# Kernel tuning notes

Measured on AMD Instinct MI355X. Metric: run time of the kernel, lower is better.

Reference implementation:

```python
import jax, jax.numpy as jnp
import numpy as np
import math

VOCAB, D, L, NC, DC, K, DFF = 50257, 1024, 8, 4096, 256, 8, 4096
B, T = 8, 256

def ternary_ste(w):
    # torch: w_q + (w - w_q).detach() -> forward value == w, grad only via w_q
    alpha = jnp.maximum(jnp.mean(jnp.abs(w)), 1e-5)
    w_q = jnp.clip(jnp.round(w / alpha), -1.0, 1.0)
    return w_q + jax.lax.stop_gradient(w - w_q)

def rmsnorm(x, w):
    return x * jax.lax.rsqrt(jnp.mean(x * x, axis=-1, keepdims=True) + 1e-6) * w

def setup_inputs() -> dict:
    key = jax.random.key(0)
    ks = jax.random.split(key, 16)
    n = lambda k, sh, s: (jax.random.normal(k, sh, dtype=jnp.float32) * s)
    return {
        'tokens': jax.random.randint(ks[0], (B, T), 0, VOCAB),
        'embed': n(ks[1], (VOCAB, D), 0.02),
        'ln_in_w': jnp.ones((D,), jnp.float32),
        'ln_out_w': jnp.ones((D,), jnp.float32),
        'W_route': n(ks[2], (L, NC, D), 0.02),
        'cells': n(ks[3], (L, NC, DC), 0.01),
        'W_in': n(ks[4], (L, D, DC), 0.01),
        'W_out': n(ks[5], (L, DC, D), 0.01),
        'state_decay': jnp.full((L,), 3.0, jnp.float32),
        'state_gate_w': jnp.full((L, D), 0.1, jnp.float32),
        'state_gate_b': jnp.zeros((L, D), jnp.float32),
        'state_scale': jnp.full((L, D), 0.1, jnp.float32),
        'cell_scale': jnp.full((L,), 0.1, jnp.float32),
        'W_ff_gate': n(ks[6], (L, D, DFF), 0.02),
        'W_ff_up': n(ks[7], (L, D, DFF), 0.02),
        'W_ff_down': n(ks[8], (L, DFF, D), 0.02),
        'ff_norm_w': jnp.ones((L, D), jnp.float32),
        'norm_w': jnp.ones((L, D), jnp.float32),
    }

def _layer(x, Wr, cells, Wi, Wo, sd, sgw, sgb, ss, cs, Wg, Wu, Wd, ffn_w, nrm_w):
    Bx, Tx, Dx = x.shape
    # cell memory
    scores = jnp.einsum('btd,cd->btc', x, ternary_ste(Wr)) / math.sqrt(Dx)
    topk_s, topk_i = jax.lax.top_k(scores, K)          # [B,T,K]
    w = jax.nn.softmax(topk_s, axis=-1)
    cell_vals = cells[topk_i]                          # [B,T,K,DC]
    readout = jnp.einsum('btkc,btk->btc', cell_vals, w)
    x_in = jnp.einsum('btd,dc->btc', x, ternary_ste(Wi))
    cell_out = jnp.einsum('btc,cd->btd', readout + x_in, ternary_ste(Wo))
    # running state scan
    gate = jax.nn.sigmoid(x * sgw + sgb)
    updates = gate * x                                  # [B,T,D]
    decay = jnp.clip(jax.nn.sigmoid(sd), 0.01, 0.99)
    def step(h, u):
        h = h * decay + u
        return h, h
    _, states = jax.lax.scan(step, jnp.zeros((Bx, Dx), x.dtype), jnp.swapaxes(updates, 0, 1))
    state_out = jnp.swapaxes(states, 0, 1) * ss
    x = rmsnorm(x + cs * cell_out + state_out, nrm_w)
    # ternary SwiGLU FFN
    h = rmsnorm(x, ffn_w)
    g = jnp.einsum('btd,df->btf', h, ternary_ste(Wg))
    u = jnp.einsum('btd,df->btf', h, ternary_ste(Wu))
    ff = jnp.einsum('btf,fd->btd', jax.nn.silu(g) * u, ternary_ste(Wd))
    return x + ff

def reference(tokens, embed, ln_in_w, ln_out_w, W_route, cells, W_in, W_out,
              state_decay, state_gate_w, state_gate_b, state_scale, cell_scale,
              W_ff_gate, W_ff_up, W_ff_down, ff_norm_w, norm_w):
    h = rmsnorm(embed[tokens], ln_in_w)
    for i in range(L):
        h = _layer(h, W_route[i], cells[i], W_in[i], W_out[i], state_decay[i],
                   state_gate_w[i], state_gate_b[i], state_scale[i], cell_scale[i],
                   W_ff_gate[i], W_ff_up[i], W_ff_down[i], ff_norm_w[i], norm_w[i])
    logits = jnp.einsum('btd,vd->btv', rmsnorm(h, ln_out_w), embed)  # tied head
    return logits
```

## Files before the change

### kernel.cpp

```cpp
#include <hip/hip_runtime.h>
#include <stdint.h>

typedef __attribute__((ext_vector_type(8))) short bf16x8;
typedef __attribute__((ext_vector_type(4))) float f32x4;
typedef unsigned short u16;
typedef unsigned int u32;

#define MTOK 2048
#define DMODEL 1024
#define NCELL 4096
#define DCELL 256
#define DFF 4096
#define NVOCAB 50257
#define VPAD_LD 50304

static __device__ __forceinline__ u16 f2bf(float f) {
  u32 u = __builtin_bit_cast(u32, f);
  u = (u + 0x7FFFu + ((u >> 16) & 1u)) >> 16;
  return (u16)u;
}
static __device__ __forceinline__ u32 pk2(float a, float b) {
  return (u32)f2bf(a) | ((u32)f2bf(b) << 16);
}
static __device__ __forceinline__ float sigm(float x) { return 1.0f / (1.0f + __expf(-x)); }

static __device__ __forceinline__ void glds16(const void* g, void* l) {
  __builtin_amdgcn_global_load_lds(
      (const __attribute__((address_space(1))) void*)g,
      (__attribute__((address_space(3))) void*)l, 16, 0, 0);
}

static __device__ __forceinline__ float blockReduceSum(float v) {
#pragma unroll
  for (int o = 32; o > 0; o >>= 1) v += __shfl_xor(v, o);
  __shared__ float sm[4];
  __syncthreads();
  if ((threadIdx.x & 63) == 0) sm[threadIdx.x >> 6] = v;
  __syncthreads();
  return sm[0] + sm[1] + sm[2] + sm[3];
}

static __device__ __forceinline__ void blockReducePair1024(
    float& a, float& b, float* sm)
{
#pragma unroll
  for (int o = 32; o > 0; o >>= 1) { a += __shfl_xor(a, o); b += __shfl_xor(b, o); }
  int wv = threadIdx.x >> 6;
  if ((threadIdx.x & 63) == 0) { sm[wv * 2] = a; sm[wv * 2 + 1] = b; }
  __syncthreads();
  float ra = 0.f, rb = 0.f;
#pragma unroll
  for (int i = 0; i < 16; ++i) { ra += sm[i * 2]; rb += sm[i * 2 + 1]; }
  __syncthreads();
  a = ra; b = rb;
}

template<int TM, int TN, int EPI>
static __device__ __forceinline__ void v3_body(
    int bid, int T, char* smem,
    const u16* A, const u16* B,
    float* Cf, u16* Cb, const float* Res,
    int NB, int K, int ldc, float alpha)
{
  u16* As = (u16*)smem;
  u16* Bs = (u16*)(smem + TM * 128);
  constexpr int MI = TM / 32;
  constexpr int NI = TN / 32;
  constexpr int ACH = TM / 32;
  constexpr int BCH = TN / 32;
  constexpr int MB = 2048 / TM;
  const int tid = threadIdx.x;
  const int w = (bid & 7) * (T >> 3) + (bid >> 3);
  const int m0 = (w % MB) * TM;
  const int n0 = (w / MB) * TN;
  const int l = tid & 63;
  const int wv = tid >> 6;
  const int wm = wv >> 1, wn = wv & 1;
  const int lr = l & 15, lg = l >> 4;
  const int wbase = tid & ~63;

  f32x4 acc[MI][NI] = {};

  const int row_ = tid >> 3;
  const int kc_ = (tid & 7) << 3;
  const int nk = K >> 6;

  for (int s = 0; s < nk; ++s) {
    const int k0 = s << 6;
#pragma unroll
    for (int c = 0; c < ACH; ++c) {
      int row = c * 32 + row_;
      glds16(&A[(size_t)(m0 + row) * K + k0 + kc_],
             &As[(size_t)(c * 256 + wbase) * 8]);
    }
#pragma unroll
    for (int c = 0; c < BCH; ++c) {
      int row = c * 32 + row_;
      int gr = n0 + row; if (gr > NB - 1) gr = NB - 1;
      glds16(&B[(size_t)gr * K + k0 + kc_],
             &Bs[(size_t)(c * 256 + wbase) * 8]);
    }
    __syncthreads();
#pragma unroll
    for (int kk = 0; kk < 2; ++kk) {
      bf16x8 fa[MI], fb[NI];
#pragma unroll
      for (int mi = 0; mi < MI; ++mi)
        fa[mi] = *(const bf16x8*)&As[(wm * (TM / 2) + mi * 16 + lr) * 64 + kk * 32 + lg * 8];
#pragma unroll
      for (int ni = 0; ni < NI; ++ni)
        fb[ni] = *(const bf16x8*)&Bs[(wn * (TN / 2) + ni * 16 + lr) * 64 + kk * 32 + lg * 8];
#pragma unroll
      for (int mi = 0; mi < MI; ++mi)
#pragma unroll
        for (int ni = 0; ni < NI; ++ni)
          acc[mi][ni] = __builtin_amdgcn_mfma_f32_16x16x32_bf16(fa[mi], fb[ni], acc[mi][ni], 0, 0, 0);
    }
    __syncthreads();
  }

#pragma unroll
  for (int mi = 0; mi < MI; ++mi)
#pragma unroll
    for (int ni = 0; ni < NI; ++ni) {
      int col = n0 + wn * (TN / 2) + ni * 16 + lr;
#pragma unroll
      for (int j = 0; j < 4; ++j) {
        int row = m0 + wm * (TM / 2) + mi * 16 + lg * 4 + j;
        float v = acc[mi][ni][j];
        if constexpr (EPI == 0) {
          Cf[(size_t)row * ldc + col] = v * alpha;
        } else if constexpr (EPI == 1) {
          size_t off = (size_t)row * ldc + col;
          float r = Res[off] + v;
          Cf[off] = r;
          Cb[off] = f2bf(r);
        } else if constexpr (EPI == 2) {
          if (col < NB) Cf[(size_t)row * ldc + col] = v;
        } else if constexpr (EPI == 3) {
          float p = __shfl_xor(v, 1);
          float a = v * sigm(v) * p;
          float a2 = __shfl_xor(a, 2);
          if ((lr & 3) == 0)
            *(u32*)&Cb[(size_t)row * DFF + (col >> 1)] = pk2(a, a2);
        } else {
          __builtin_nontemporal_store(v, &Cf[(size_t)row * ldc + col]);
        }
      }
    }
}

template<int TM, int TN, int EPI>
__global__ __launch_bounds__(256, 3) void k_gemm_v3(
    const u16* __restrict__ A, const u16* __restrict__ B,
    float* __restrict__ Cf, u16* __restrict__ Cb, const float* __restrict__ Res,
    int NB, int K, int ldc, float alpha)
{
  __shared__ __align__(16) char smem[(TM + TN) * 128];
  v3_body<TM, TN, EPI>(blockIdx.x, gridDim.x, smem, A, B, Cf, Cb, Res,
                       NB, K, ldc, alpha);
}

static __device__ __forceinline__ void transpose_body(
    int bid, char* smem,
    const float* Wi, const float* Wo, const float* Wg, const float* Wu,
    const float* Wd, const float* Wr,
    u16* WiT, u16* WoT, u16* WguT, u16* WdT, u16* WrB)
{
  if (bid >= 12800) {
    int i = (bid - 12800) * 256 + threadIdx.x;
    const float4* s = (const float4*)(Wr + (size_t)i * 8);
    float4 a = s[0], b = s[1];
    *(uint4*)(WrB + (size_t)i * 8) =
        make_uint4(pk2(a.x, a.y), pk2(a.z, a.w), pk2(b.x, b.y), pk2(b.z, b.w));
    return;
  }
  const float* src; u16* dst; int R, C, t0, mul, add;
  if (bid < 256)       { src = Wi; dst = WiT;  R = 1024; C = 256;  t0 = bid;        mul = 1; add = 0; }
  else if (bid < 512)  { src = Wo; dst = WoT;  R = 256;  C = 1024; t0 = bid - 256;  mul = 1; add = 0; }
  else if (bid < 4608) { src = Wg; dst = WguT; R = 1024; C = 4096; t0 = bid - 512;  mul = 2; add = 0; }
  else if (bid < 8704) { src = Wu; dst = WguT; R = 1024; C = 4096; t0 = bid - 4608; mul = 2; add = 1; }
  else                 { src = Wd; dst = WdT;  R = 4096; C = 1024; t0 = bid - 8704; mul = 1; add = 0; }
  int tC = C >> 5;
  int r0 = (t0 / tC) << 5, c0 = (t0 % tC) << 5;
  float (*tile)[33] = (float(*)[33])smem;
  int ty = threadIdx.x >> 3;
  int tx = (threadIdx.x & 7) << 2;
  float4 v = *(const float4*)&src[(size_t)(r0 + ty) * C + c0 + tx];
  tile[ty][tx] = v.x; tile[ty][tx + 1] = v.y; tile[ty][tx + 2] = v.z; tile[ty][tx + 3] = v.w;
  __syncthreads();
  float a = tile[tx][ty], b = tile[tx + 1][ty], c = tile[tx + 2][ty], d = tile[tx + 3][ty];
  *(uint2*)&dst[((size_t)(c0 + ty) * mul + add) * R + r0 + tx] = make_uint2(pk2(a, b), pk2(c, d));
}

__global__ void k_transpose_layer(
    const float* __restrict__ Wi, const float* __restrict__ Wo,
    const float* __restrict__ Wg, const float* __restrict__ Wu,
    const float* __restrict__ Wd, const float* __restrict__ Wr,
    u16* __restrict__ WiT, u16* __restrict__ WoT,
    u16* __restrict__ WguT, u16* __restrict__ WdT, u16* __restrict__ WrB)
{
  __shared__ __align__(16) char smem[4224];
  transpose_body(blockIdx.x, smem, Wi, Wo, Wg, Wu, Wd, Wr,
                 WiT, WoT, WguT, WdT, WrB);
}

static __device__ __forceinline__ void gemm64_body(
    const u16* A, const u16* B, float* Cf,
    int m0, int n0, int K, int lda, int ldb, int ldc, char* smem)
{
  u16* As = (u16*)smem;
  u16* Bs = (u16*)(smem + 64 * 64 * 2);
  const int tid = threadIdx.x;
  const int l = tid & 63;
  const int wv = tid >> 6;
  const int wm = wv >> 1, wn = wv & 1;
  const int lr = l & 15, lg = l >> 4;

  uint4 aR[2], bR[2];
  f32x4 acc[2][2] = {};
  const int nk = K >> 6;

  auto loadAB = [&](int k0) {
#pragma unroll
    for (int c = 0; c < 2; ++c) {
      int id = c * 256 + tid;
      int row = id >> 3, kc = (id & 7) << 3;
      aR[c] = *(const uint4*)&A[(size_t)(m0 + row) * lda + k0 + kc];
      bR[c] = *(const uint4*)&B[(size_t)(n0 + row) * ldb + k0 + kc];
    }
  };
  auto stage = [&]() {
#pragma unroll
    for (int c = 0; c < 2; ++c) {
      int id = c * 256 + tid;
      int row = id >> 3, kc = (id & 7) << 3;
      *(uint4*)&As[row * 64 + kc] = aR[c];
      *(uint4*)&Bs[row * 64 + kc] = bR[c];
    }
  };

  loadAB(0);
  for (int s = 0; s < nk; ++s) {
    __syncthreads();
    stage();
    __syncthreads();
    if (s + 1 < nk) loadAB((s + 1) << 6);
#pragma unroll
    for (int kk = 0; kk < 2; ++kk) {
      bf16x8 fa[2], fb[2];
#pragma unroll
      for (int mi = 0; mi < 2; ++mi)
        fa[mi] = *(const bf16x8*)&As[(wm * 32 + mi * 16 + lr) * 64 + kk * 32 + lg * 8];
#pragma unroll
      for (int ni = 0; ni < 2; ++ni)
        fb[ni] = *(const bf16x8*)&Bs[(wn * 32 + ni * 16 + lr) * 64 + kk * 32 + lg * 8];
#pragma unroll
      for (int mi = 0; mi < 2; ++mi)
#pragma unroll
        for (int ni = 0; ni < 2; ++ni)
          acc[mi][ni] = __builtin_amdgcn_mfma_f32_16x16x32_bf16(fa[mi], fb[ni], acc[mi][ni], 0, 0, 0);
    }
  }

#pragma unroll
  for (int mi = 0; mi < 2; ++mi)
#pragma unroll
    for (int ni = 0; ni < 2; ++ni) {
      int col = n0 + wn * 32 + ni * 16 + lr;
#pragma unroll
      for (int j = 0; j < 4; ++j) {
        int row = m0 + wm * 32 + mi * 16 + lg * 4 + j;
        Cf[(size_t)row * ldc + col] = acc[mi][ni][j];
      }
    }
}

__global__ __launch_bounds__(256, 3) void k_gemm64(
    const u16* __restrict__ A, const u16* __restrict__ B,
    float* __restrict__ Cf, int K, int lda, int ldb, int ldc)
{
  __shared__ __align__(16) char smem[16384];
  gemm64_body(A, B, Cf, blockIdx.x * 64, blockIdx.y * 64, K, lda, ldb, ldc, smem);
}

__global__ __launch_bounds__(256, 3) void k_head_fused(
    const u16* __restrict__ x_bf, const u16* __restrict__ WrB,
    float* __restrict__ scores,
    const u16* __restrict__ WiT, float* __restrict__ xin,
    const float* __restrict__ x_f, float* __restrict__ E,
    const float* __restrict__ sgw, const float* __restrict__ sgb,
    const float* __restrict__ sdec)
{
  __shared__ __align__(16) char smem[32768];
  int bid = blockIdx.x;
  if (bid < 512) {
    v3_body<128, 128, 0>(bid, 512, smem, x_bf, WrB, scores, nullptr, nullptr,
                         NCELL, DMODEL, NCELL, 0.03125f);
    return;
  }
  if (bid < 640) {
    int b2 = bid - 512;
    gemm64_body(x_bf, WiT, xin, (b2 & 31) * 64, (b2 >> 5) * 64,
                DMODEL, DMODEL, DMODEL, DCELL, smem);
    return;
  }
  int tid = (bid - 640) * 256 + threadIdx.x;
  int d = tid & 1023, bc = tid >> 10;
  int b = bc >> 4, c = bc & 15;
  float dec = sigm(sdec[0]);
  dec = fminf(fmaxf(dec, 0.01f), 0.99f);
  float gw = sgw[d], gb = sgb[d];
  size_t base = ((size_t)b * 256 + c * 16) * DMODEL + d;
  float h = 0.f;
  for (int t = 0; t < 16; ++t) {
    float xv = x_f[base + (size_t)t * DMODEL];
    h = h * dec + sigm(xv * gw + gb) * xv;
  }
  E[tid] = h;
}

__global__ __launch_bounds__(256, 3) void k_wd_prep(
    const u16* __restrict__ act, const u16* __restrict__ WdT_cur,
    float* __restrict__ x_f, u16* __restrict__ x_bf,
    const float* __restrict__ Wi, const float* __restrict__ Wo,
    const float* __restrict__ Wg, const float* __restrict__ Wu,
    const float* __restrict__ Wd, const float* __restrict__ Wr,
    u16* __restrict__ WiT, u16* __restrict__ WoT,
    u16* __restrict__ WguT, u16* __restrict__ WdT_nxt, u16* __restrict__ WrB)
{
  __shared__ __align__(16) char smem[16384];
  int bid = blockIdx.x;
  if (bid < 512) {
    v3_body<64, 64, 1>(bid, 512, smem, act, WdT_cur, x_f, x_bf, x_f,
                       DMODEL, DFF, DMODEL, 1.0f);
  } else {
    transpose_body(bid - 512, smem, Wi, Wo, Wg, Wu, Wd, Wr,
                   WiT, WoT, WguT, WdT_nxt, WrB);
  }
}

__global__ __launch_bounds__(256) void k_copy_out(
    const float* __restrict__ pad, float* __restrict__ out)
{
  int row = blockIdx.x;
  const float* s = pad + (size_t)row * VPAD_LD;
  float* d = out + (size_t)row * NVOCAB;
  int t = threadIdx.x;
  int head = (int)((16 - (((size_t)d) & 15)) & 15) >> 2;
  if (t < head) d[t] = s[t];
  int nb = (NVOCAB - head) >> 2;
  const float* sb = s + head;
  float* db = d + head;
  for (int i = t; i < nb; i += 256) {
    f32x4 v;
    v.x = __builtin_nontemporal_load(&sb[i * 4 + 0]);
    v.y = __builtin_nontemporal_load(&sb[i * 4 + 1]);
    v.z = __builtin_nontemporal_load(&sb[i * 4 + 2]);
    v.w = __builtin_nontemporal_load(&sb[i * 4 + 3]);
    __builtin_nontemporal_store(v, (f32x4*)&db[i * 4]);
  }
  int t0 = head + nb * 4;
  int rem = NVOCAB - t0;
  if (t < rem) d[t0 + t] = s[t0 + t];
}

__global__ __launch_bounds__(256) void k_cell_fused(
    const float* __restrict__ scores, const float* __restrict__ cells,
    const float* __restrict__ xin, u16* __restrict__ rb)
{
  __shared__ float sw[4][8];
  __shared__ int si[4][8];
  int row0 = blockIdx.x * 4;
  int wvid = threadIdx.x >> 6;
  int row = row0 + wvid;
  int l = threadIdx.x & 63;
  const float* s = scores + (size_t)row * NCELL;
  float v[8]; int ix[8];
#pragma unroll
  for (int i = 0; i < 8; ++i) { v[i] = -3.4e38f; ix[i] = 0x7fffffff; }
  for (int j = 0; j < 64; ++j) {
    float x = s[j * 64 + l];
    if (x > v[7]) {
      v[7] = x; ix[7] = j * 64 + l;
#pragma unroll
      for (int q = 7; q > 0; --q) {
        if (v[q] > v[q - 1]) {
          float tv = v[q]; v[q] = v[q - 1]; v[q - 1] = tv;
          int tt = ix[q]; ix[q] = ix[q - 1]; ix[q - 1] = tt;
        }
      }
    }
  }
  float ov[8]; int oi[8];
#pragma unroll
  for (int r = 0; r < 8; ++r) {
    float bv = v[0]; int bi = ix[0];
#pragma unroll
    for (int o = 32; o > 0; o >>= 1) {
      float tv = __shfl_xor(bv, o);
      int tb = __shfl_xor(bi, o);
      if (tv > bv || (tv == bv && tb < bi)) { bv = tv; bi = tb; }
    }
    ov[r] = bv; oi[r] = bi;
    if (bi == ix[0]) {
#pragma unroll
      for (int q = 0; q < 7; ++q) { v[q] = v[q + 1]; ix[q] = ix[q + 1]; }
      v[7] = -3.4e38f; ix[7] = 0x7fffffff;
    }
  }
  if (l == 0) {
    float m = ov[0], sum = 0.f, e[8];
#pragma unroll
    for (int r = 0; r < 8; ++r) { e[r] = __expf(ov[r] - m); sum += e[r]; }
    float inv = 1.0f / sum;
#pragma unroll
    for (int r = 0; r < 8; ++r) { sw[wvid][r] = e[r] * inv; si[wvid][r] = oi[r]; }
  }
  __syncthreads();
  int d = threadIdx.x;
#pragma unroll
  for (int r = 0; r < 4; ++r) {
    int rr = row0 + r;
    float acc = xin[(size_t)rr * DCELL + d];
#pragma unroll
    for (int k = 0; k < 8; ++k)
      acc += sw[r][k] * cells[(size_t)si[r][k] * DCELL + d];
    rb[(size_t)rr * DCELL + d] = f2bf(acc);
  }
}

__global__ __launch_bounds__(1024) void k_scan_norm(
    float* __restrict__ x_f, const float* __restrict__ co,
    const float* __restrict__ E, u16* __restrict__ h2b,
    const float* __restrict__ sgw, const float* __restrict__ sgb,
    const float* __restrict__ ssc, const float* __restrict__ sdec,
    const float* __restrict__ csc, const float* __restrict__ nw,
    const float* __restrict__ fw)
{
  __shared__ float sm[32];
  int b = blockIdx.x >> 4, c = blockIdx.x & 15;
  int d = threadIdx.x;
  float dec = sigm(sdec[0]);
  dec = fminf(fmaxf(dec, 0.01f), 0.99f);
  float d2 = dec * dec, d4 = d2 * d2, d8 = d4 * d4;
  float d16 = d8 * d8;
  float cs = csc[0];
  float gw = sgw[d], gb = sgb[d], sc = ssc[d];
  float nwd = nw[d], fwd = fw[d];
  float h = 0.f;
  for (int cc = 0; cc < c; ++cc) h = h * d16 + E[((b << 4) + cc) * 1024 + d];
  size_t base = ((size_t)b * 256 + c * 16) * DMODEL + d;
  for (int t = 0; t < 16; ++t) {
    size_t o = base + (size_t)t * DMODEL;
    float xv = x_f[o];
    float g = sigm(xv * gw + gb);
    h = h * dec + g * xv;
    float pre = xv + cs * co[o] + h * sc;
    float pn = pre * nwd;
    float s1 = pre * pre, s2 = pn * pn;
    blockReducePair1024(s1, s2, sm);
    float inv = rsqrtf(s1 * (1.0f / DMODEL) + 1e-6f);
    float x1 = pre * inv * nwd;
    float inv2 = rsqrtf(inv * inv * s2 * (1.0f / DMODEL) + 1e-6f);
    x_f[o] = x1;
    h2b[o] = f2bf(x1 * inv2 * fwd);
  }
}

__global__ void k_embed_norm(const int* __restrict__ tok, const float* __restrict__ emb,
                             const float* __restrict__ w, float* __restrict__ xf,
                             u16* __restrict__ xb)
{
  int row = blockIdx.x;
  int t = tok[row];
  float4 v = ((const float4*)(emb + (size_t)t * DMODEL))[threadIdx.x];
  float tot = blockReduceSum(v.x * v.x + v.y * v.y + v.z * v.z + v.w * v.w);
  float inv = rsqrtf(tot * (1.0f / DMODEL) + 1e-6f);
  int d0 = threadIdx.x << 2;
  float4 wv = *(const float4*)(w + d0);
  float4 o;
  o.x = v.x * inv * wv.x; o.y = v.y * inv * wv.y;
  o.z = v.z * inv * wv.z; o.w = v.w * inv * wv.w;
  *(float4*)(xf + (size_t)row * DMODEL + d0) = o;
  *(uint2*)(xb + (size_t)row * DMODEL + d0) = make_uint2(pk2(o.x, o.y), pk2(o.z, o.w));
}

__global__ __launch_bounds__(256) void k_tail(
    const float* __restrict__ xf, const float* __restrict__ w,
    u16* __restrict__ ob, const float* __restrict__ emb,
    u16* __restrict__ emb_bf)
{
  int bid = blockIdx.x;
  if (bid >= 2048) {
    int i = (bid - 2048) * 256 + threadIdx.x;
    if (i >= NVOCAB * (DMODEL / 8)) return;
    const float4* s = (const float4*)(emb + (size_t)i * 8);
    float4 a = s[0], b = s[1];
    *(uint4*)(emb_bf + (size_t)i * 8) =
        make_uint4(pk2(a.x, a.y), pk2(a.z, a.w), pk2(b.x, b.y), pk2(b.z, b.w));
    return;
  }
  int row = bid;
  float4 v = ((const float4*)(xf + (size_t)row * DMODEL))[threadIdx.x];
  float tot = blockReduceSum(v.x * v.x + v.y * v.y + v.z * v.z + v.w * v.w);
  float inv = rsqrtf(tot * (1.0f / DMODEL) + 1e-6f);
  int d0 = threadIdx.x << 2;
  float4 wv = *(const float4*)(w + d0);
  *(uint2*)(ob + (size_t)row * DMODEL + d0) =
      make_uint2(pk2(v.x * inv * wv.x, v.y * inv * wv.y),
                 pk2(v.z * inv * wv.z, v.w * inv * wv.w));
}

extern "C" void kernel_launch(void* const* d_in, const int* in_sizes, int n_in,
                              void* d_out, int out_size, void* d_ws, size_t ws_size,
                              hipStream_t stream)
{
  const int*   tokens  = (const int*)d_in[0];
  const float* embed   = (const float*)d_in[1];
  const float* ln_in_w = (const float*)d_in[2];
  const float* ln_out_w= (const float*)d_in[3];
  const float* W_route = (const float*)d_in[4];
  const float* cells   = (const float*)d_in[5];
  const float* W_in    = (const float*)d_in[6];
  const float* W_out   = (const float*)d_in[7];
  const float* sdec    = (const float*)d_in[8];
  const float* sgw     = (const float*)d_in[9];
  const float* sgb     = (const float*)d_in[10];
  const float* ssc     = (const float*)d_in[11];
  const float* csc     = (const float*)d_in[12];
  const float* Wg      = (const float*)d_in[13];
  const float* Wu      = (const float*)d_in[14];
  const float* Wd      = (const float*)d_in[15];
  const float* ffw     = (const float*)d_in[16];
  const float* nrw     = (const float*)d_in[17];
  float* out = (float*)d_out;
  (void)in_sizes; (void)n_in; (void)out_size;

  char* ws = (char*)d_ws;
  size_t off = 0;
  auto alloc = [&](size_t bytes) -> void* {
    void* p = ws + off;
    off += (bytes + 255) & ~(size_t)255;
    return p;
  };

  float* scores = (float*)alloc((size_t)MTOK * NCELL * 4);
  u16*  act_bf  = (u16*)alloc((size_t)MTOK * DFF * 2);
  float* x_f    = (float*)alloc((size_t)MTOK * DMODEL * 4);
  u16*  x_bf    = (u16*)alloc((size_t)MTOK * DMODEL * 2);
  u16*  h2_bf   = (u16*)alloc((size_t)MTOK * DMODEL * 2);
  float* xin    = (float*)alloc((size_t)MTOK * DCELL * 4);
  u16*  r_bf    = (u16*)alloc((size_t)MTOK * DCELL * 2);
  float* cellout= (float*)alloc((size_t)MTOK * DMODEL * 4);
  u16*  WiT     = (u16*)alloc((size_t)DCELL * DMODEL * 2);
  u16*  WoT     = (u16*)alloc((size_t)DMODEL * DCELL * 2);
  u16*  WguT    = (u16*)alloc((size_t)8192 * DMODEL * 2);
  u16*  WdTa    = (u16*)alloc((size_t)DMODEL * DFF * 2);
  u16*  WdTb    = (u16*)alloc((size_t)DMODEL * DFF * 2);
  u16*  WrB     = (u16*)alloc((size_t)NCELL * DMODEL * 2);
  float* E      = (float*)alloc((size_t)131072 * 4);
  if (off < ((size_t)108 << 20)) off = (size_t)108 << 20;
  u16*  xf_bf   = (u16*)alloc((size_t)MTOK * DMODEL * 2);
  float* vpad   = (float*)alloc((size_t)MTOK * VPAD_LD * 4);
  size_t need_pad = off;
  u16*  embed_bf = (u16*)ws;

  const bool use_pad = (ws_size >= need_pad);

  k_embed_norm<<<MTOK, 256, 0, stream>>>(tokens, embed, ln_in_w, x_f, x_bf);
  k_transpose_layer<<<14848, 256, 0, stream>>>(W_in, W_out, Wg, Wu, Wd, W_route,
                                               WiT, WoT, WguT, WdTa, WrB);

  for (int lay = 0; lay < 8; ++lay) {
    const float* cells_l = cells + (size_t)lay * NCELL * DCELL;
    u16* WdT_cur = (lay & 1) ? WdTb : WdTa;
    u16* WdT_nxt = (lay & 1) ? WdTa : WdTb;

    k_head_fused<<<1152, 256, 0, stream>>>(x_bf, WrB, scores, WiT, xin, x_f, E,
        sgw + lay * DMODEL, sgb + lay * DMODEL, sdec + lay);
    k_cell_fused<<<512, 256, 0, stream>>>(scores, cells_l, xin, r_bf);
    k_gemm64<<<dim3(32, 16), 256, 0, stream>>>(r_bf, WoT, cellout,
        DCELL, DCELL, DCELL, DMODEL);
    k_scan_norm<<<128, 1024, 0, stream>>>(x_f, cellout, E, h2_bf,
        sgw + lay * DMODEL, sgb + lay * DMODEL, ssc + lay * DMODEL,
        sdec + lay, csc + lay, nrw + lay * DMODEL, ffw + lay * DMODEL);
    k_gemm_v3<128, 128, 3><<<1024, 256, 0, stream>>>(h2_bf, WguT, nullptr, act_bf,
        nullptr, 8192, DMODEL, 0, 1.0f);
    if (lay < 7) {
      int nl = lay + 1;
      k_wd_prep<<<15360, 256, 0, stream>>>(act_bf, WdT_cur, x_f, x_bf,
          W_in  + (size_t)nl * DMODEL * DCELL,
          W_out + (size_t)nl * DCELL * DMODEL,
          Wg    + (size_t)nl * DMODEL * DFF,
          Wu    + (size_t)nl * DMODEL * DFF,
          Wd    + (size_t)nl * DFF * DMODEL,
          W_route + (size_t)nl * NCELL * DMODEL,
          WiT, WoT, WguT, WdT_nxt, WrB);
    } else {
      k_gemm_v3<64, 64, 1><<<512, 256, 0, stream>>>(act_bf, WdT_cur, x_f, x_bf,
          x_f, DMODEL, DFF, DMODEL, 1.0f);
    }
  }

  k_tail<<<2048 + 25129, 256, 0, stream>>>(x_f, ln_out_w, xf_bf, embed, embed_bf);
  if (use_pad) {
    k_gemm_v3<128, 128, 4><<<6288, 256, 0, stream>>>(xf_bf, embed_bf, vpad, nullptr,
        nullptr, NVOCAB, DMODEL, VPAD_LD, 1.0f);
    k_copy_out<<<MTOK, 256, 0, stream>>>(vpad, out);
  } else {
    k_gemm_v3<128, 128, 2><<<6288, 256, 0, stream>>>(xf_bf, embed_bf, out, nullptr,
        nullptr, NVOCAB, DMODEL, NVOCAB, 1.0f);
  }
}
```

Baseline: 2.485 ms.

## Spread embedding bf16 conversion across layers and store padded logits as bf16

The fp32-to-bf16 conversion of the tied embedding table is split into eight chunks and folded into the per-layer Wd/prep kernel, so it runs alongside each layer's down-projection GEMM instead of in one tail kernel. The head GEMM's padded output is now written as packed bf16 instead of fp32, and the copy-out kernel widens it back to fp32. This halves the padded intermediate traffic, but it rounds the logits to bf16 precision, which may fail tolerance checks. The embedding copy now needs a dedicated workspace buffer, and the last layer's Wd GEMM goes through the fused kernel.

After: 2.587 ms. 1.04x slower.

```diff
diff --git a/kernel.cpp b/kernel.cpp
--- a/kernel.cpp
+++ b/kernel.cpp
@@ -13,6 +13,9 @@
 #define DFF 4096
 #define NVOCAB 50257
 #define VPAD_LD 50304
+#define NCONV8 (NVOCAB * 128)
+#define CONV_CHUNK (NCONV8 / 8)
+#define CONV_BLOCKS ((CONV_CHUNK + 255) / 256)
 
 static __device__ __forceinline__ u16 f2bf(float f) {
   u32 u = __builtin_bit_cast(u32, f);
@@ -53,6 +56,15 @@
   for (int i = 0; i < 16; ++i) { ra += sm[i * 2]; rb += sm[i * 2 + 1]; }
   __syncthreads();
   a = ra; b = rb;
+}
+
+static __device__ __forceinline__ void conv_group(
+    int i, const float* emb, u16* emb_bf)
+{
+  const float4* s = (const float4*)(emb + (size_t)i * 8);
+  float4 a = s[0], b = s[1];
+  *(uint4*)(emb_bf + (size_t)i * 8) =
+      make_uint4(pk2(a.x, a.y), pk2(a.z, a.w), pk2(b.x, b.y), pk2(b.z, b.w));
 }
 
 template<int TM, int TN, int EPI>
@@ -144,7 +156,10 @@
           if ((lr & 3) == 0)
             *(u32*)&Cb[(size_t)row * DFF + (col >> 1)] = pk2(a, a2);
         } else {
-          __builtin_nontemporal_store(v, &Cf[(size_t)row * ldc + col]);
+          float p = __shfl_xor(v, 1);
+          if ((lr & 1) == 0)
+            __builtin_nontemporal_store(pk2(v, p),
+                (u32*)&Cb[(size_t)row * ldc + col]);
         }
       }
     }
@@ -169,10 +184,7 @@
 {
   if (bid >= 12800) {
     int i = (bid - 12800) * 256 + threadIdx.x;
-    const float4* s = (const float4*)(Wr + (size_t)i * 8);
-    float4 a = s[0], b = s[1];
-    *(uint4*)(WrB + (size_t)i * 8) =
-        make_uint4(pk2(a.x, a.y), pk2(a.z, a.w), pk2(b.x, b.y), pk2(b.z, b.w));
+    conv_group(i, Wr, WrB);
     return;
   }
   const float* src; u16* dst; int R, C, t0, mul, add;
@@ -327,42 +339,56 @@
     const float* __restrict__ Wg, const float* __restrict__ Wu,
     const float* __restrict__ Wd, const float* __restrict__ Wr,
     u16* __restrict__ WiT, u16* __restrict__ WoT,
-    u16* __restrict__ WguT, u16* __restrict__ WdT_nxt, u16* __restrict__ WrB)
+    u16* __restrict__ WguT, u16* __restrict__ WdT_nxt, u16* __restrict__ WrB,
+    int prep, const float* __restrict__ emb, u16* __restrict__ emb_bf,
+    int conv_base, int conv_end)
 {
   __shared__ __align__(16) char smem[16384];
   int bid = blockIdx.x;
   if (bid < 512) {
     v3_body<64, 64, 1>(bid, 512, smem, act, WdT_cur, x_f, x_bf, x_f,
                        DMODEL, DFF, DMODEL, 1.0f);
-  } else {
+    return;
+  }
+  if (bid < 512 + prep) {
     transpose_body(bid - 512, smem, Wi, Wo, Wg, Wu, Wd, Wr,
                    WiT, WoT, WguT, WdT_nxt, WrB);
-  }
-}
-
-__global__ __launch_bounds__(256) void k_copy_out(
-    const float* __restrict__ pad, float* __restrict__ out)
+    return;
+  }
+  int i = conv_base + (bid - 512 - prep) * 256 + threadIdx.x;
+  if (i < conv_end) conv_group(i, emb, emb_bf);
+}
+
+__global__ __launch_bounds__(256) void k_copy_out_bf(
+    const u16* __restrict__ pad, float* __restrict__ out)
 {
   int row = blockIdx.x;
-  const float* s = pad + (size_t)row * VPAD_LD;
+  const u32* s = (const u32*)(pad + (size_t)row * VPAD_LD);
   float* d = out + (size_t)row * NVOCAB;
   int t = threadIdx.x;
-  int head = (int)((16 - (((size_t)d) & 15)) & 15) >> 2;
-  if (t < head) d[t] = s[t];
-  int nb = (NVOCAB - head) >> 2;
-  const float* sb = s + head;
-  float* db = d + head;
-  for (int i = t; i < nb; i += 256) {
-    f32x4 v;
-    v.x = __builtin_nontemporal_load(&sb[i * 4 + 0]);
-    v.y = __builtin_nontemporal_load(&sb[i * 4 + 1]);
-    v.z = __builtin_nontemporal_load(&sb[i * 4 + 2]);
-    v.w = __builtin_nontemporal_load(&sb[i * 4 + 3]);
-    __builtin_nontemporal_store(v, (f32x4*)&db[i * 4]);
-  }
-  int t0 = head + nb * 4;
-  int rem = NVOCAB - t0;
-  if (t < rem) d[t0 + t] = s[t0 + t];
+  const int n4 = NVOCAB >> 2;
+  bool al = ((row & 3) == 0);
+  for (int i = t; i < n4; i += 256) {
+    u32 w0 = __builtin_nontemporal_load(&s[i * 2 + 0]);
+    u32 w1 = __builtin_nontemporal_load(&s[i * 2 + 1]);
+    f32x4 f;
+    f.x = __builtin_bit_cast(float, w0 << 16);
+    f.y = __builtin_bit_cast(float, w0 & 0xFFFF0000u);
+    f.z = __builtin_bit_cast(float, w1 << 16);
+    f.w = __builtin_bit_cast(float, w1 & 0xFFFF0000u);
+    if (al) {
+      __builtin_nontemporal_store(f, (f32x4*)&d[i * 4]);
+    } else {
+      __builtin_nontemporal_store(f.x, &d[i * 4 + 0]);
+      __builtin_nontemporal_store(f.y, &d[i * 4 + 1]);
+      __builtin_nontemporal_store(f.z, &d[i * 4 + 2]);
+      __builtin_nontemporal_store(f.w, &d[i * 4 + 3]);
+    }
+  }
+  if (t == 0) {
+    u16 w = pad[(size_t)row * VPAD_LD + n4 * 4];
+    d[n4 * 4] = __builtin_bit_cast(float, (u32)w << 16);
+  }
 }
 
 __global__ __launch_bounds__(256) void k_cell_fused(
@@ -486,7 +512,22 @@
   *(uint2*)(xb + (size_t)row * DMODEL + d0) = make_uint2(pk2(o.x, o.y), pk2(o.z, o.w));
 }
 
-__global__ __launch_bounds__(256) void k_tail(
+__global__ __launch_bounds__(256) void k_tail_norm(
+    const float* __restrict__ xf, const float* __restrict__ w,
+    u16* __restrict__ ob)
+{
+  int row = blockIdx.x;
+  float4 v = ((const float4*)(xf + (size_t)row * DMODEL))[threadIdx.x];
+  float tot = blockReduceSum(v.x * v.x + v.y * v.y + v.z * v.z + v.w * v.w);
+  float inv = rsqrtf(tot * (1.0f / DMODEL) + 1e-6f);
+  int d0 = threadIdx.x << 2;
+  float4 wv = *(const float4*)(w + d0);
+  *(uint2*)(ob + (size_t)row * DMODEL + d0) =
+      make_uint2(pk2(v.x * inv * wv.x, v.y * inv * wv.y),
+                 pk2(v.z * inv * wv.z, v.w * inv * wv.w));
+}
+
+__global__ __launch_bounds__(256) void k_tail_full(
     const float* __restrict__ xf, const float* __restrict__ w,
     u16* __restrict__ ob, const float* __restrict__ emb,
     u16* __restrict__ emb_bf)
@@ -494,11 +535,8 @@
   int bid = blockIdx.x;
   if (bid >= 2048) {
     int i = (bid - 2048) * 256 + threadIdx.x;
-    if (i >= NVOCAB * (DMODEL / 8)) return;
-    const float4* s = (const float4*)(emb + (size_t)i * 8);
-    float4 a = s[0], b = s[1];
-    *(uint4*)(emb_bf + (size_t)i * 8) =
-        make_uint4(pk2(a.x, a.y), pk2(a.z, a.w), pk2(b.x, b.y), pk2(b.z, b.w));
+    if (i >= NCONV8) return;
+    conv_group(i, emb, emb_bf);
     return;
   }
   int row = bid;
@@ -560,13 +598,13 @@
   u16*  WdTb    = (u16*)alloc((size_t)DMODEL * DFF * 2);
   u16*  WrB     = (u16*)alloc((size_t)NCELL * DMODEL * 2);
   float* E      = (float*)alloc((size_t)131072 * 4);
-  if (off < ((size_t)108 << 20)) off = (size_t)108 << 20;
   u16*  xf_bf   = (u16*)alloc((size_t)MTOK * DMODEL * 2);
-  float* vpad   = (float*)alloc((size_t)MTOK * VPAD_LD * 4);
-  size_t need_pad = off;
-  u16*  embed_bf = (u16*)ws;
-
-  const bool use_pad = (ws_size >= need_pad);
+  u16*  embed_ded = (u16*)alloc((size_t)NVOCAB * DMODEL * 2);
+  u16*  vpad      = (u16*)alloc((size_t)MTOK * VPAD_LD * 2);
+  size_t need = off;
+
+  const bool use_pad = (ws_size >= need);
+  u16* embed_bf = use_pad ? embed_ded : (u16*)ws;
 
   k_embed_norm<<<MTOK, 256, 0, stream>>>(tokens, embed, ln_in_w, x_f, x_bf);
   k_transpose_layer<<<14848, 256, 0, stream>>>(W_in, W_out, Wg, Wu, Wd, W_route,
@@ -587,28 +625,30 @@
         sdec + lay, csc + lay, nrw + lay * DMODEL, ffw + lay * DMODEL);
     k_gemm_v3<128, 128, 3><<<1024, 256, 0, stream>>>(h2_bf, WguT, nullptr, act_bf,
         nullptr, 8192, DMODEL, 0, 1.0f);
-    if (lay < 7) {
-      int nl = lay + 1;
-      k_wd_prep<<<15360, 256, 0, stream>>>(act_bf, WdT_cur, x_f, x_bf,
-          W_in  + (size_t)nl * DMODEL * DCELL,
-          W_out + (size_t)nl * DCELL * DMODEL,
-          Wg    + (size_t)nl * DMODEL * DFF,
-          Wu    + (size_t)nl * DMODEL * DFF,
-          Wd    + (size_t)nl * DFF * DMODEL,
-          W_route + (size_t)nl * NCELL * DMODEL,
-          WiT, WoT, WguT, WdT_nxt, WrB);
-    } else {
-      k_gemm_v3<64, 64, 1><<<512, 256, 0, stream>>>(act_bf, WdT_cur, x_f, x_bf,
-          x_f, DMODEL, DFF, DMODEL, 1.0f);
-    }
-  }
-
-  k_tail<<<2048 + 25129, 256, 0, stream>>>(x_f, ln_out_w, xf_bf, embed, embed_bf);
+    int prep = (lay < 7) ? 14848 : 0;
+    int conv_n = use_pad ? CONV_BLOCKS : 0;
+    int conv_base = lay * CONV_CHUNK;
+    int conv_end = (lay == 7) ? NCONV8 : (conv_base + CONV_CHUNK);
+    int nl = (lay < 7) ? (lay + 1) : lay;
+    k_wd_prep<<<512 + prep + conv_n, 256, 0, stream>>>(act_bf, WdT_cur, x_f, x_bf,
+        W_in  + (size_t)nl * DMODEL * DCELL,
+        W_out + (size_t)nl * DCELL * DMODEL,
+        Wg    + (size_t)nl * DMODEL * DFF,
+        Wu    + (size_t)nl * DMODEL * DFF,
+        Wd    + (size_t)nl * DFF * DMODEL,
+        W_route + (size_t)nl * NCELL * DMODEL,
+        WiT, WoT, WguT, WdT_nxt, WrB,
+        prep, embed, embed_bf, conv_base, conv_end);
+  }
+
   if (use_pad) {
-    k_gemm_v3<128, 128, 4><<<6288, 256, 0, stream>>>(xf_bf, embed_bf, vpad, nullptr,
-        nullptr, NVOCAB, DMODEL, VPAD_LD, 1.0f);
-    k_copy_out<<<MTOK, 256, 0, stream>>>(vpad, out);
+    k_tail_norm<<<MTOK, 256, 0, stream>>>(x_f, ln_out_w, xf_bf);
+    k_gemm_v3<128, 128, 5><<<6288, 256, 0, stream>>>(xf_bf, embed_bf, nullptr,
+        vpad, nullptr, NVOCAB, DMODEL, VPAD_LD, 1.0f);
+    k_copy_out_bf<<<MTOK, 256, 0, stream>>>(vpad, out);
   } else {
+    k_tail_full<<<2048 + 25129, 256, 0, stream>>>(x_f, ln_out_w, xf_bf,
+        embed, embed_bf);
     k_gemm_v3<128, 128, 2><<<6288, 256, 0, stream>>>(xf_bf, embed_bf, out, nullptr,
         nullptr, NVOCAB, DMODEL, NVOCAB, 1.0f);
   }
```
